# Kernel optimization log

Hardware: AMD Instinct MI355X
Metric: run time of the kernel (lower is better)

Reference implementation:

```python
import jax, jax.numpy as jnp
import numpy as np


def _laplacian(x, edge_src, edge_dst, n_nodes):
    # x: [B, N, C]; L[:, i, :] = x[:, i, :] - mean over neighbors j of x[:, j, :]
    # (nodes with zero neighbors get L = 0, matching the torch loop which skips them)
    xt = jnp.transpose(x, (1, 0, 2))                      # [N, B, C]
    gathered = xt[edge_src]                               # [E, B, C]
    neigh_sum = jax.ops.segment_sum(gathered, edge_dst, num_segments=n_nodes)  # [N, B, C]
    deg = jax.ops.segment_sum(jnp.ones_like(edge_dst, dtype=x.dtype), edge_dst,
                              num_segments=n_nodes)       # [N]
    safe_deg = jnp.maximum(deg, 1.0)
    neigh_mean = neigh_sum / safe_deg[:, None, None]
    lap = jnp.where(deg[:, None, None] > 0, xt - neigh_mean, jnp.zeros((), x.dtype))
    return jnp.transpose(lap, (1, 0, 2))                  # [B, N, C]


def setup_inputs() -> dict:
    key = jax.random.key(0)
    k1, k2, k3, k4 = jax.random.split(key, 4)
    B, N, C = 4, 100000, 32
    E = 1600000  # avg degree 16
    pred = jax.random.normal(k1, (B, N, C), dtype=jnp.float32)
    target = jax.random.normal(k2, (B, N, C), dtype=jnp.float32)
    edge_src = jax.random.randint(k3, (E,), 0, N, dtype=jnp.int32)
    edge_dst = jax.random.randint(k4, (E,), 0, N, dtype=jnp.int32)
    return {"pred": pred, "target": target, "edge_src": edge_src, "edge_dst": edge_dst}


def reference(pred, target, edge_src, edge_dst):
    n_nodes = pred.shape[1]
    lap_pred = _laplacian(pred, edge_src, edge_dst, n_nodes)
    lap_target = _laplacian(target, edge_src, edge_dst, n_nodes)
    # nn.L1Loss() default reduction='mean' over all elements
    return jnp.mean(jnp.abs(lap_pred - lap_target))
```

## Files before the change

kernel.cpp:

```cpp
#include <hip/hip_runtime.h>
#include <hip/hip_bf16.h>

#define BB 4
#define CC 32

#define KMAX   512
#define STRIDE 4608

#if __has_builtin(__builtin_amdgcn_cvt_pk_f32_bf8) && __has_builtin(__builtin_amdgcn_cvt_pk_bf8_f32)
#define HW_BF8 1
typedef float f2v __attribute__((ext_vector_type(2)));
#else
#define HW_BF8 0
#endif

__device__ __forceinline__ unsigned pack_bf2(float x, float y) {
    unsigned bx = __float_as_uint(x); bx += 0x7fffu + ((bx >> 16) & 1u);
    unsigned by = __float_as_uint(y); by += 0x7fffu + ((by >> 16) & 1u);
    return (bx >> 16) | (by & 0xffff0000u);
}

__device__ __forceinline__ unsigned pack_e5(float x) {
    _Float16 h = (_Float16)x;
    unsigned hb = (unsigned)__builtin_bit_cast(unsigned short, h);
    hb += 0x7fu + ((hb >> 8) & 1u);
    return (hb >> 8) & 0xffu;
}

__device__ __forceinline__ float e5h(unsigned hw) {
    return (float)__builtin_bit_cast(_Float16, (unsigned short)hw);
}

__device__ __forceinline__ unsigned pack_e5x4(float d0, float d1, float d2, float d3) {
#if HW_BF8
    int w = __builtin_amdgcn_cvt_pk_bf8_f32(d0, d1, 0, false);
    w     = __builtin_amdgcn_cvt_pk_bf8_f32(d2, d3, w, true);
    return (unsigned)w;
#else
    return pack_e5(d0) | (pack_e5(d1) << 8) | (pack_e5(d2) << 16) | (pack_e5(d3) << 24);
#endif
}

__device__ __forceinline__ void acc_e5(float* acc, uint2 v) {
#if HW_BF8
    f2v p0 = __builtin_amdgcn_cvt_pk_f32_bf8((int)v.x, false);
    f2v p1 = __builtin_amdgcn_cvt_pk_f32_bf8((int)v.x, true);
    f2v p2 = __builtin_amdgcn_cvt_pk_f32_bf8((int)v.y, false);
    f2v p3 = __builtin_amdgcn_cvt_pk_f32_bf8((int)v.y, true);
    acc[0] += p0[0]; acc[1] += p0[1];
    acc[2] += p1[0]; acc[3] += p1[1];
    acc[4] += p2[0]; acc[5] += p2[1];
    acc[6] += p3[0]; acc[7] += p3[1];
#else
    unsigned a = v.x, b = v.y;
    acc[0] += e5h((a << 8) & 0xff00u);
    acc[1] += e5h(a & 0xff00u);
    acc[2] += e5h((a >> 8) & 0xff00u);
    acc[3] += e5h((a >> 16) & 0xff00u);
    acc[4] += e5h((b << 8) & 0xff00u);
    acc[5] += e5h(b & 0xff00u);
    acc[6] += e5h((b >> 8) & 0xff00u);
    acc[7] += e5h((b >> 16) & 0xff00u);
#endif
}

__global__ __launch_bounds__(1024) void prep_a(
        const float* __restrict__ pred, const float* __restrict__ target,
        const int* __restrict__ edge_src, const int* __restrict__ edge_dst,
        int* __restrict__ bucketCursor, unsigned* __restrict__ staged,
        unsigned* __restrict__ diffu, unsigned* __restrict__ diffu8,
        int N, int E, int buildBlocks, int K) {
    if ((int)blockIdx.x < buildBlocks) {
        __shared__ int cnt[KMAX];
        __shared__ int base[KMAX];
        for (int k = threadIdx.x; k < K; k += 1024) cnt[k] = 0;
        __syncthreads();
        int e0 = blockIdx.x * 8192;
        unsigned w[8]; int rp[8];
        #pragma unroll
        for (int t = 0; t < 8; ++t) {
            int i = e0 + t * 1024 + threadIdx.x;
            if (i < E) {
                int d = __builtin_nontemporal_load(&edge_dst[i]);
                int s = __builtin_nontemporal_load(&edge_src[i]);
                int bk = d >> 8;
                w[t] = (unsigned)s | ((unsigned)(d & 255) << 17);
                int r = atomicAdd(&cnt[bk], 1);
                rp[t] = r | (bk << 13);
            } else rp[t] = -1;
        }
        __syncthreads();
        for (int k = threadIdx.x; k < K; k += 1024) {
            int c = cnt[k];
            base[k] = c ? atomicAdd(&bucketCursor[k], c) : 0;
        }
        __syncthreads();
        #pragma unroll
        for (int t = 0; t < 8; ++t) {
            if (rp[t] >= 0) {
                int bk  = rp[t] >> 13;
                int pos = base[bk] + (rp[t] & 8191);
                if (pos < STRIDE)
                    staged[(size_t)bk * STRIDE + pos] = w[t];
            }
        }
    } else {
        int idx4 = ((int)blockIdx.x - buildBlocks) * 1024 + threadIdx.x;
        int total4 = N * CC;
        if (idx4 < total4) {
            int n8 = N * 8;
            int b  = idx4 / n8;
            int r  = idx4 - b * n8;
            int n  = r >> 3;
            const float4 p = *(const float4*)(pred   + ((size_t)idx4 << 2));
            const float4 t = *(const float4*)(target + ((size_t)idx4 << 2));
            float d0 = p.x - t.x, d1 = p.y - t.y, d2 = p.z - t.z, d3 = p.w - t.w;
            uint2 u;
            u.x = pack_bf2(d0, d1);
            u.y = pack_bf2(d2, d3);
            *(uint2*)(diffu + (size_t)n * 64 + b * 16 + ((r & 7) << 1)) = u;
            diffu8[(size_t)n * 32 + b * 8 + (r & 7)] = pack_e5x4(d0, d1, d2, d3);
        }
    }
}

__global__ __launch_bounds__(256) void node_gather(
        const unsigned* __restrict__ diffu, const unsigned* __restrict__ diffu8,
        const unsigned* __restrict__ staged,
        const int* __restrict__ bucketCursor, float* __restrict__ partials, int N) {
    __shared__ int lists[64 * 65];
    __shared__ int cnt[64];
    __shared__ float wpart[4];

    int bk  = blockIdx.x >> 2;
    int sub = blockIdx.x & 3;
    if (threadIdx.x < 64) cnt[threadIdx.x] = 0;
    __syncthreads();

    int count = min(bucketCursor[bk], STRIDE);
    const unsigned* sb = staged + (size_t)bk * STRIDE;
    for (int i = threadIdx.x; i < count; i += 256) {
        unsigned wv = sb[i];
        int loc = (wv >> 17) & 255;
        if ((loc >> 6) == sub) {
            int l = loc & 63;
            int slot = atomicAdd(&cnt[l], 1);
            if (slot < 64) lists[l * 65 + slot] = wv & 0x1ffff;
        }
    }
    __syncthreads();

    int wave = threadIdx.x >> 6;
    int lane = threadIdx.x & 63;
    int q  = lane >> 4;
    int l4 = lane & 15;
    const unsigned* base16 = diffu  + l4 * 4;
    const unsigned* base8  = diffu8 + l4 * 2;
    int node0 = (bk << 8) + (sub << 6);
    float total = 0.0f;

    for (int tt = 0; tt < 4; ++tt) {
        int lslot = (wave << 4) + (tt << 2) + q;
        int node  = node0 + lslot;
        int d = (node < N) ? min(cnt[lslot], 64) : 0;
        if (d > 0) {
            int dm1   = d - 1;
            int lbase = lslot * 65;
            uint4 su = *(const uint4*)(base16 + (size_t)node * 64);

            float accA[8], accB[8];
            #pragma unroll
            for (int k = 0; k < 8; ++k) { accA[k] = 0.f; accB[k] = 0.f; }

            for (int j = 0; j < d; j += 4) {
                int s0 = lists[lbase + j];
                int s1 = lists[lbase + min(j + 1, dm1)];
                int s2 = lists[lbase + min(j + 2, dm1)];
                int s3 = lists[lbase + min(j + 3, dm1)];
                uint2 v0 = *(const uint2*)(base8 + (size_t)s0 * 32);
                uint2 v1 = *(const uint2*)(base8 + (size_t)s1 * 32);
                uint2 v2 = *(const uint2*)(base8 + (size_t)s2 * 32);
                uint2 v3 = *(const uint2*)(base8 + (size_t)s3 * 32);
                acc_e5(accA, v0);
                if (j + 1 < d) acc_e5(accB, v1);
                if (j + 2 < d) acc_e5(accA, v2);
                if (j + 3 < d) acc_e5(accB, v3);
            }

            float inv = 1.0f / (float)d;
            const unsigned* sp = (const unsigned*)&su;
            #pragma unroll
            for (int k = 0; k < 8; ++k) {
                float v = accA[k] + accB[k];
                unsigned spk = sp[k >> 1];
                float s = (k & 1) ? __uint_as_float(spk & 0xffff0000u)
                                  : __uint_as_float(spk << 16);
                total += fabsf(s - v * inv);
            }
        }
    }
    #pragma unroll
    for (int delta = 32; delta >= 1; delta >>= 1)
        total += __shfl_down(total, delta, 64);
    if (lane == 0) wpart[wave] = total;
    __syncthreads();
    if (threadIdx.x == 0)
        partials[blockIdx.x] = wpart[0] + wpart[1] + wpart[2] + wpart[3];
}

__global__ __launch_bounds__(256) void reduce_kernel(const float* __restrict__ partials, int n,
                                                     float* __restrict__ out, float inv_count) {
    float s = 0.0f;
    for (int i = threadIdx.x; i < n; i += 256) s += partials[i];
    int lane = threadIdx.x & 63;
    int wave = threadIdx.x >> 6;
    #pragma unroll
    for (int delta = 32; delta >= 1; delta >>= 1)
        s += __shfl_down(s, delta, 64);
    __shared__ float wpart[4];
    if (lane == 0) wpart[wave] = s;
    __syncthreads();
    if (threadIdx.x == 0)
        out[0] = (wpart[0] + wpart[1] + wpart[2] + wpart[3]) * inv_count;
}

__global__ void build_kernel(const int* __restrict__ edge_src, const int* __restrict__ edge_dst,
                             int* __restrict__ deg, int* __restrict__ csr, int E) {
    int i = blockIdx.x * 256 + threadIdx.x;
    if (i < E) {
        int d = edge_dst[i];
        int slot = atomicAdd(&deg[d], 1);
        if (slot < 64) csr[(d << 6) + slot] = edge_src[i];
    }
}

__global__ __launch_bounds__(256) void node_kernel_pt(const float* __restrict__ pred,
                                                      const float* __restrict__ target,
                                                      const int* __restrict__ csr,
                                                      const int* __restrict__ deg,
                                                      float* __restrict__ partials, int N) {
    int wave = threadIdx.x >> 6;
    int lane = threadIdx.x & 63;
    int node = blockIdx.x * 4 + wave;
    float total = 0.0f;
    if (node < N) {
        int d = min(deg[node], 64);
        if (d > 0) {
            int o = node << 6;
            int cs = csr[o + lane];
            int b = (lane >> 3) & 3;
            int q = lane & 7;
            const float* arr = (lane >= 32) ? target : pred;
            int rowbase = b * N * CC + q * 4;
            float4 sp = *(const float4*)(pred + rowbase + node * CC);
            float4 st = *(const float4*)(target + rowbase + node * CC);
            float ax = 0.f, ay = 0.f, az = 0.f, aw = 0.f;
            for (int j = 0; j < d; ++j) {
                int s = __shfl(cs, j, 64);
                float4 v = *(const float4*)(arr + rowbase + s * CC);
                ax += v.x; ay += v.y; az += v.z; aw += v.w;
            }
            float dx = ax - __shfl_down(ax, 32, 64);
            float dy = ay - __shfl_down(ay, 32, 64);
            float dz = az - __shfl_down(az, 32, 64);
            float dw = aw - __shfl_down(aw, 32, 64);
            if (lane < 32) {
                float inv = 1.0f / (float)d;
                total = fabsf((sp.x - st.x) - dx * inv)
                      + fabsf((sp.y - st.y) - dy * inv)
                      + fabsf((sp.z - st.z) - dz * inv)
                      + fabsf((sp.w - st.w) - dw * inv);
            }
        }
    }
    #pragma unroll
    for (int delta = 32; delta >= 1; delta >>= 1)
        total += __shfl_down(total, delta, 64);
    __shared__ float wpart[4];
    if (lane == 0) wpart[wave] = total;
    __syncthreads();
    if (threadIdx.x == 0)
        partials[blockIdx.x] = wpart[0] + wpart[1] + wpart[2] + wpart[3];
}

extern "C" void kernel_launch(void* const* d_in, const int* in_sizes, int n_in,
                              void* d_out, int out_size, void* d_ws, size_t ws_size,
                              hipStream_t stream) {
    const float* pred   = (const float*)d_in[0];
    const float* target = (const float*)d_in[1];
    const int* edge_src = (const int*)d_in[2];
    const int* edge_dst = (const int*)d_in[3];
    float* out = (float*)d_out;

    const int BNC = in_sizes[0];
    const int E   = in_sizes[2];
    const int N   = BNC / (BB * CC);
    const int K   = (N + 255) >> 8;

    size_t staged_off = 512;
    size_t diff_off   = staged_off + (size_t)K * STRIDE;
    diff_off = (diff_off + 3) & ~(size_t)3;
    size_t diff8_off  = diff_off + ((size_t)N << 6);
    size_t part_off   = diff8_off + ((size_t)N << 5);
    size_t fast_bytes = (part_off + (size_t)4 * K + 16) * 4;

    if (ws_size >= fast_bytes && N <= 131072 && K <= KMAX) {
        int* cursor = (int*)d_ws;
        unsigned* staged = (unsigned*)((int*)d_ws + staged_off);
        unsigned* diffu  = (unsigned*)((int*)d_ws + diff_off);
        unsigned* diffu8 = (unsigned*)((int*)d_ws + diff8_off);
        float* partials  = (float*)((int*)d_ws + part_off);

        hipMemsetAsync(cursor, 0, 512 * sizeof(int), stream);
        const int buildBlocks = (E + 8191) / 8192;
        const int diffBlocks  = (N * CC + 1023) / 1024;
        prep_a<<<buildBlocks + diffBlocks, 1024, 0, stream>>>(
            pred, target, edge_src, edge_dst, cursor, staged, diffu, diffu8,
            N, E, buildBlocks, K);
        node_gather<<<4 * K, 256, 0, stream>>>(diffu, diffu8, staged, cursor,
                                               partials, N);
        reduce_kernel<<<1, 256, 0, stream>>>(partials, 4 * K, out, 1.0f / (float)BNC);
    } else {
        int* deg = (int*)d_ws;
        int* csr = deg + N;
        float* partials = (float*)(csr + ((size_t)N << 6));
        const int nblocks4 = (N + 3) / 4;

        hipMemsetAsync(deg, 0, (size_t)N * sizeof(int), stream);
        const int eblocks = (E + 255) / 256;
        build_kernel<<<eblocks, 256, 0, stream>>>(edge_src, edge_dst, deg, csr, E);
        node_kernel_pt<<<nblocks4, 256, 0, stream>>>(pred, target, csr, deg, partials, N);
        reduce_kernel<<<1, 256, 0, stream>>>(partials, nblocks4, out, 1.0f / (float)BNC);
    }
}
```

Measured before the change: 187.7 us.

## Bucket edges by 64-node sub-buckets so each gather block reads only its own edges

The edge bucketing in prep_a now uses 64-node sub-buckets (dst>>6) instead of 256-node buckets, with a per-sub-bucket cursor and a stride computed from the average load plus slack. Each node_gather block then scans only the edges for its own 64 nodes, instead of all four sub-blocks rereading the whole 256-node bucket and discarding three quarters of it. This cuts the staged-edge read traffic and filter work in the gather, at the cost of four times as many shared-memory counters and global cursor atomics in the build phase. It also replaces the nontemporal loads of edge indices with plain loads.

```diff
diff --git a/kernel.cpp b/kernel.cpp
--- a/kernel.cpp
+++ b/kernel.cpp
@@ -1,11 +1,12 @@
 #include <hip/hip_runtime.h>
 #include <hip/hip_bf16.h>
+#include <cmath>
 
 #define BB 4
 #define CC 32
 
 #define KMAX   512
-#define STRIDE 4608
+#define NSUBMAX (KMAX * 4)
 
 #if __has_builtin(__builtin_amdgcn_cvt_pk_f32_bf8) && __has_builtin(__builtin_amdgcn_cvt_pk_bf8_f32)
 #define HW_BF8 1
@@ -69,11 +70,12 @@
         const int* __restrict__ edge_src, const int* __restrict__ edge_dst,
         int* __restrict__ bucketCursor, unsigned* __restrict__ staged,
         unsigned* __restrict__ diffu, unsigned* __restrict__ diffu8,
-        int N, int E, int buildBlocks, int K) {
+        int N, int E, int buildBlocks, int K, int sstride) {
     if ((int)blockIdx.x < buildBlocks) {
-        __shared__ int cnt[KMAX];
-        __shared__ int base[KMAX];
-        for (int k = threadIdx.x; k < K; k += 1024) cnt[k] = 0;
+        __shared__ int cnt[NSUBMAX];
+        __shared__ int base[NSUBMAX];
+        int nsub = K << 2;
+        for (int k = threadIdx.x; k < nsub; k += 1024) cnt[k] = 0;
         __syncthreads();
         int e0 = blockIdx.x * 8192;
         unsigned w[8]; int rp[8];
@@ -81,16 +83,16 @@
         for (int t = 0; t < 8; ++t) {
             int i = e0 + t * 1024 + threadIdx.x;
             if (i < E) {
-                int d = __builtin_nontemporal_load(&edge_dst[i]);
-                int s = __builtin_nontemporal_load(&edge_src[i]);
-                int bk = d >> 8;
-                w[t] = (unsigned)s | ((unsigned)(d & 255) << 17);
-                int r = atomicAdd(&cnt[bk], 1);
-                rp[t] = r | (bk << 13);
+                int d = edge_dst[i];
+                int s = edge_src[i];
+                int sbk = d >> 6;
+                w[t] = (unsigned)s | ((unsigned)(d & 63) << 17);
+                int r = atomicAdd(&cnt[sbk], 1);
+                rp[t] = r | (sbk << 13);
             } else rp[t] = -1;
         }
         __syncthreads();
-        for (int k = threadIdx.x; k < K; k += 1024) {
+        for (int k = threadIdx.x; k < nsub; k += 1024) {
             int c = cnt[k];
             base[k] = c ? atomicAdd(&bucketCursor[k], c) : 0;
         }
@@ -98,10 +100,10 @@
         #pragma unroll
         for (int t = 0; t < 8; ++t) {
             if (rp[t] >= 0) {
-                int bk  = rp[t] >> 13;
-                int pos = base[bk] + (rp[t] & 8191);
-                if (pos < STRIDE)
-                    staged[(size_t)bk * STRIDE + pos] = w[t];
+                int sbk = rp[t] >> 13;
+                int pos = base[sbk] + (rp[t] & 8191);
+                if (pos < sstride)
+                    staged[(size_t)sbk * sstride + pos] = w[t];
             }
         }
     } else {
@@ -127,26 +129,23 @@
 __global__ __launch_bounds__(256) void node_gather(
         const unsigned* __restrict__ diffu, const unsigned* __restrict__ diffu8,
         const unsigned* __restrict__ staged,
-        const int* __restrict__ bucketCursor, float* __restrict__ partials, int N) {
+        const int* __restrict__ bucketCursor, float* __restrict__ partials,
+        int N, int sstride) {
     __shared__ int lists[64 * 65];
     __shared__ int cnt[64];
     __shared__ float wpart[4];
 
-    int bk  = blockIdx.x >> 2;
-    int sub = blockIdx.x & 3;
+    int subg = blockIdx.x;
     if (threadIdx.x < 64) cnt[threadIdx.x] = 0;
     __syncthreads();
 
-    int count = min(bucketCursor[bk], STRIDE);
-    const unsigned* sb = staged + (size_t)bk * STRIDE;
+    int count = min(bucketCursor[subg], sstride);
+    const unsigned* sb = staged + (size_t)subg * sstride;
     for (int i = threadIdx.x; i < count; i += 256) {
         unsigned wv = sb[i];
-        int loc = (wv >> 17) & 255;
-        if ((loc >> 6) == sub) {
-            int l = loc & 63;
-            int slot = atomicAdd(&cnt[l], 1);
-            if (slot < 64) lists[l * 65 + slot] = wv & 0x1ffff;
-        }
+        int l = (wv >> 17) & 63;
+        int slot = atomicAdd(&cnt[l], 1);
+        if (slot < 64) lists[l * 65 + slot] = wv & 0x1ffff;
     }
     __syncthreads();
 
@@ -156,7 +155,7 @@
     int l4 = lane & 15;
     const unsigned* base16 = diffu  + l4 * 4;
     const unsigned* base8  = diffu8 + l4 * 2;
-    int node0 = (bk << 8) + (sub << 6);
+    int node0 = subg << 6;
     float total = 0.0f;
 
     for (int tt = 0; tt < 4; ++tt) {
@@ -296,13 +295,17 @@
     const int E   = in_sizes[2];
     const int N   = BNC / (BB * CC);
     const int K   = (N + 255) >> 8;
-
-    size_t staged_off = 512;
-    size_t diff_off   = staged_off + (size_t)K * STRIDE;
+    const int nsub = 4 * K;
+
+    const int msub = E / nsub + 1;
+    const int sstride = msub + 8 * (int)sqrtf((float)msub) + 64;
+
+    size_t staged_off = NSUBMAX;
+    size_t diff_off   = staged_off + (size_t)nsub * sstride;
     diff_off = (diff_off + 3) & ~(size_t)3;
     size_t diff8_off  = diff_off + ((size_t)N << 6);
     size_t part_off   = diff8_off + ((size_t)N << 5);
-    size_t fast_bytes = (part_off + (size_t)4 * K + 16) * 4;
+    size_t fast_bytes = (part_off + (size_t)nsub + 16) * 4;
 
     if (ws_size >= fast_bytes && N <= 131072 && K <= KMAX) {
         int* cursor = (int*)d_ws;
@@ -311,15 +314,15 @@
         unsigned* diffu8 = (unsigned*)((int*)d_ws + diff8_off);
         float* partials  = (float*)((int*)d_ws + part_off);
 
-        hipMemsetAsync(cursor, 0, 512 * sizeof(int), stream);
+        hipMemsetAsync(cursor, 0, NSUBMAX * sizeof(int), stream);
         const int buildBlocks = (E + 8191) / 8192;
         const int diffBlocks  = (N * CC + 1023) / 1024;
         prep_a<<<buildBlocks + diffBlocks, 1024, 0, stream>>>(
             pred, target, edge_src, edge_dst, cursor, staged, diffu, diffu8,
-            N, E, buildBlocks, K);
-        node_gather<<<4 * K, 256, 0, stream>>>(diffu, diffu8, staged, cursor,
-                                               partials, N);
-        reduce_kernel<<<1, 256, 0, stream>>>(partials, 4 * K, out, 1.0f / (float)BNC);
+            N, E, buildBlocks, K, sstride);
+        node_gather<<<nsub, 256, 0, stream>>>(diffu, diffu8, staged, cursor,
+                                              partials, N, sstride);
+        reduce_kernel<<<1, 256, 0, stream>>>(partials, nsub, out, 1.0f / (float)BNC);
     } else {
         int* deg = (int*)d_ws;
         int* csr = deg + N;
```

After: 187.2 us, median of 2. No clear change (-0.2%).
